# Optimization experiments

Hardware: AMD Instinct MI355X
Metric: run time of the kernel (lower is better)

## Reference

```python
import jax, jax.numpy as jnp
import numpy as np
from jax import lax

B, S, T = 16, 256, 800
V, D, M, H = 256, 512, 80, 1024
NH = 4; HD = D // NH; EH = 256  # encoder LSTM hidden per direction


def setup_inputs() -> dict:
    key = jax.random.key(0)
    it = iter(jax.random.split(key, 40))
    def rn(shape, s=0.05):
        return jax.random.normal(next(it), shape, jnp.float32) * s
    return dict(
        text_inputs=jax.random.randint(next(it), (B, S), 0, V),
        mel_targets=jax.random.normal(next(it), (B, T, M), jnp.float32),
        emb=rn((V, D), 0.1),
        conv_w=rn((3, D, D, 5)), conv_b=rn((3, D)),
        bn_gamma=jnp.ones((3, D)), bn_beta=jnp.zeros((3, D)),
        bn_mean=rn((3, D)), bn_var=jnp.ones((3, D)),
        enc_Wih_f=rn((4 * EH, D)), enc_Whh_f=rn((4 * EH, EH)), enc_b_f=rn((4 * EH,)),
        enc_Wih_b=rn((4 * EH, D)), enc_Whh_b=rn((4 * EH, EH)), enc_b_b=rn((4 * EH,)),
        Wq=rn((D, M)), bq=rn((D,)), Wk=rn((D, D)), bk=rn((D,)),
        Wv=rn((D, D)), bv=rn((D,)), Wo=rn((D, D)), bo=rn((D,)),
        dec_Wih1=rn((4 * H, D + M)), dec_b1=rn((4 * H,)),
        dec_Wih2=rn((4 * H, H)), dec_b2=rn((4 * H,)),
        mel_W=rn((M, H)), mel_b=rn((M,)),
        stop_W=rn((1, H)), stop_b=rn((1,)),
    )


def _lstm_cell_zero(x, Wih, b):
    # single-step LSTM cell from zero (h, c); original resets state every timestep
    g = x @ Wih.T + b
    i, f, gg, o = jnp.split(g, 4, axis=-1)
    c = jax.nn.sigmoid(i) * jnp.tanh(gg)  # c0 = 0 -> forget gate contributes nothing
    return jax.nn.sigmoid(o) * jnp.tanh(c)


def _lstm_scan(xs, Wih, Whh, b, hdim, reverse):
    # xs: (S, B, in); PyTorch gate order i,f,g,o
    def step(carry, xt):
        h, c = carry
        g = xt @ Wih.T + h @ Whh.T + b
        i, f, gg, o = jnp.split(g, 4, axis=-1)
        c = jax.nn.sigmoid(f) * c + jax.nn.sigmoid(i) * jnp.tanh(gg)
        h = jax.nn.sigmoid(o) * jnp.tanh(c)
        return (h, c), h
    z = jnp.zeros((xs.shape[1], hdim), xs.dtype)
    _, hs = lax.scan(step, (z, z), xs, reverse=reverse)
    return hs


def reference(text_inputs, mel_targets, emb, conv_w, conv_b, bn_gamma, bn_beta, bn_mean, bn_var, enc_Wih_f, enc_Whh_f, enc_b_f, enc_Wih_b, enc_Whh_b, enc_b_b, Wq, bq, Wk, bk, Wv, bv, Wo, bo, dec_Wih1, dec_b1, dec_Wih2, dec_b2, mel_W, mel_b, stop_W, stop_b):
    b_, t_, m_ = mel_targets.shape
    # ---- encoder ----
    x = emb[text_inputs].transpose(0, 2, 1)  # (B, D, S)
    for i in range(conv_w.shape[0]):
        x = lax.conv_general_dilated(x, conv_w[i], (1,), [(2, 2)], dimension_numbers=('NCH', 'OIH', 'NCH')) + conv_b[i][None, :, None]
        x = bn_gamma[i][None, :, None] * (x - bn_mean[i][None, :, None]) * lax.rsqrt(bn_var[i][None, :, None] + 1e-5) + bn_beta[i][None, :, None]
        x = jax.nn.relu(x)  # dropout in eval mode -> identity
    xs = x.transpose(2, 0, 1)  # (S, B, D)
    hf = _lstm_scan(xs, enc_Wih_f, enc_Whh_f, enc_b_f, EH, False)
    hb = _lstm_scan(xs, enc_Wih_b, enc_Whh_b, enc_b_b, EH, True)
    enc = jnp.concatenate([hf, hb], -1).transpose(1, 0, 2)  # (B, S, D)
    # ---- decoder (teacher forcing): per-step query = previous mel frame ----
    dec_in = jnp.concatenate([jnp.zeros((b_, 1, m_), mel_targets.dtype), mel_targets[:, :-1]], axis=1)  # (B, T, M)
    q = (dec_in @ Wq.T + bq).reshape(b_, t_, NH, HD)
    k = (enc @ Wk.T + bk).reshape(b_, -1, NH, HD)
    v = (enc @ Wv.T + bv).reshape(b_, -1, NH, HD)
    scores = jnp.einsum('bqhd,bkhd->bhqk', q, k) * (1.0 / np.sqrt(HD)).astype(np.float32)
    attn = jax.nn.softmax(scores, axis=-1)
    ctx = jnp.einsum('bhqk,bkhd->bqhd', attn, v).reshape(b_, t_, D) @ Wo.T + bo
    xcat = jnp.concatenate([ctx, dec_in], axis=-1)  # (B, T, D+M)
    # original re-inits decoder LSTM state each timestep -> stateless per-step cells
    h1 = _lstm_cell_zero(xcat, dec_Wih1, dec_b1)
    h2 = _lstm_cell_zero(h1, dec_Wih2, dec_b2)
    mel = h2 @ mel_W.T + mel_b      # (B, T, 80)
    stop = h2 @ stop_W.T + stop_b   # (B, T, 1) - logits (no sigmoid in training path)
    return mel, stop
```

## Files before the change

### kernel.cpp

```cpp
#include <hip/hip_runtime.h>
#include <hip/hip_bf16.h>
#include <math.h>

#define B_ 16
#define S_ 256
#define T_ 800
#define V_ 256
#define D_ 512
#define M_ 80
#define H_ 1024
#define NH_ 4
#define HD_ 128
#define EH_ 256

using bf16x8 = __attribute__((ext_vector_type(8))) short;
using f32x4  = __attribute__((ext_vector_type(4))) float;
typedef _Float16 half8 __attribute__((ext_vector_type(8)));

__device__ __forceinline__ float sigf(float x) { return 1.f / (1.f + __expf(-x)); }
__device__ __forceinline__ float tanhfast(float x) {
    float e = __expf(2.f * x);
    return 1.f - 2.f / (e + 1.f);
}

__device__ __forceinline__ unsigned short f2bf(float f) {
    unsigned int u = __float_as_uint(f);
    unsigned int r = (u + 0x7FFFu + ((u >> 16) & 1u)) >> 16;
    return (unsigned short)r;
}
__device__ __forceinline__ float bf2f(unsigned short u) {
    return __uint_as_float(((unsigned int)u) << 16);
}
__device__ __forceinline__ unsigned short h2u(_Float16 x) {
    union { _Float16 f; unsigned short u; } c; c.f = x; return c.u;
}

__device__ __forceinline__ void gl_lds16(const unsigned short* g, unsigned short* l) {
    __builtin_amdgcn_global_load_lds((const __attribute__((address_space(1))) void*)g,
                                     (__attribute__((address_space(3))) void*)l, 16, 0, 0);
}

__global__ __launch_bounds__(256) void gemm_mfma(
    const unsigned short* __restrict__ A, const unsigned short* __restrict__ Bw,
    void* __restrict__ Cv, const float* __restrict__ bias,
    int M, int N, int K, int ldc, int epi,
    const float* __restrict__ cb, const float* __restrict__ gam,
    const float* __restrict__ bet, const float* __restrict__ mu,
    const float* __restrict__ va)
{
    __shared__ unsigned short As[4096];
    __shared__ unsigned short Bs[4096];
    const int tid = threadIdx.x, w = tid >> 6, lane = tid & 63;
    const int bm = blockIdx.y * 128, bn = blockIdx.x * 128;
    const int wr = w >> 1, wc = w & 1;

    f32x4 acc[4][4];
#pragma unroll
    for (int m = 0; m < 4; ++m)
#pragma unroll
        for (int n = 0; n < 4; ++n) acc[m][n] = (f32x4){0.f, 0.f, 0.f, 0.f};

    const int r0 = w * 16 + (lane >> 2);
    const int k8 = (lane & 3) * 8;
    const unsigned short* Ag = A + (size_t)(bm + r0) * K + k8;
    const unsigned short* Bg = Bw + (size_t)(bn + r0) * K + k8;
    unsigned short* Al = As + w * 512;
    unsigned short* Bl = Bs + w * 512;

    for (int k0 = 0; k0 < K; k0 += 32) {
        __syncthreads();
        gl_lds16(Ag + k0, Al);
        gl_lds16(Ag + (size_t)64 * K + k0, Al + 2048);
        gl_lds16(Bg + k0, Bl);
        gl_lds16(Bg + (size_t)64 * K + k0, Bl + 2048);
        __syncthreads();
        bf16x8 a[4], b[4];
#pragma unroll
        for (int m = 0; m < 4; ++m)
            a[m] = *(const bf16x8*)(As + (wr * 64 + m * 16 + (lane & 15)) * 32 + (lane >> 4) * 8);
#pragma unroll
        for (int n = 0; n < 4; ++n)
            b[n] = *(const bf16x8*)(Bs + (wc * 64 + n * 16 + (lane & 15)) * 32 + (lane >> 4) * 8);
#pragma unroll
        for (int m = 0; m < 4; ++m)
#pragma unroll
            for (int n = 0; n < 4; ++n)
                acc[m][n] = __builtin_amdgcn_mfma_f32_16x16x32_bf16(a[m], b[n], acc[m][n], 0, 0, 0);
    }

    const int cr = (lane >> 4) * 4, ccol = lane & 15;
#pragma unroll
    for (int m = 0; m < 4; ++m)
#pragma unroll
        for (int n = 0; n < 4; ++n) {
            const int col = bn + wc * 64 + n * 16 + ccol;
            const float bv = (bias && !(epi == 4 && col >= 80)) ? bias[col] : 0.f;
#pragma unroll
            for (int j = 0; j < 4; ++j) {
                const int row = bm + wr * 64 + m * 16 + cr + j;
                float v = acc[m][n][j] + bv;
                if (epi == 1) {
                    float x = v + cb[col];
                    v = fmaxf(0.f, gam[col] * (x - mu[col]) * rsqrtf(va[col] + 1e-5f) + bet[col]);
                }
                if (epi == 2) {
                    ((unsigned short*)Cv)[(size_t)row * ldc + col] = f2bf(v);
                } else if (epi == 3) {
                    const int bb2 = row >> 8, ss = row & 255, hh = col >> 7, dd = col & 127;
                    ((unsigned short*)Cv)[((size_t)(bb2 * 4 + hh) * 128 + dd) * 256 + ss] = f2bf(v);
                } else if (epi == 4) {
                    if (col < 80) ((float*)Cv)[(size_t)row * ldc + col] = v;
                } else {
                    ((float*)Cv)[(size_t)row * ldc + col] = v;
                }
            }
        }
}

__global__ __launch_bounds__(256) void attn_qksm(
    const unsigned short* __restrict__ q, const unsigned short* __restrict__ k,
    unsigned short* __restrict__ probs)
{
    __shared__ unsigned short As[2048];
    __shared__ unsigned short Bs[8192];
    __shared__ float redm[64][4];
    __shared__ float reds[64][4];
    const int tid = threadIdx.x, wid = tid >> 6, lane = tid & 63;
    const int l15 = lane & 15, bq = lane >> 4;
    const int bm = blockIdx.x * 64;
    const int z = blockIdx.y, b = z >> 2, h = z & 3;

    const unsigned short* A  = q + ((size_t)b * T_) * 512 + h * 128;
    const unsigned short* Bw = k + ((size_t)b * S_) * 512 + h * 128;

    f32x4 acc[4][4];
#pragma unroll
    for (int m = 0; m < 4; ++m)
#pragma unroll
        for (int n = 0; n < 4; ++n) acc[m][n] = (f32x4){0.f, 0.f, 0.f, 0.f};

    const int r0 = wid * 16 + (lane >> 2);
    const int k8 = (lane & 3) * 8;

    for (int k0 = 0; k0 < 128; k0 += 32) {
        __syncthreads();
        gl_lds16(A + (size_t)(bm + r0) * 512 + k0 + k8, As + wid * 512);
        gl_lds16(Bw + (size_t)r0 * 512 + k0 + k8,          Bs + wid * 512);
        gl_lds16(Bw + (size_t)(64 + r0) * 512 + k0 + k8,   Bs + 2048 + wid * 512);
        gl_lds16(Bw + (size_t)(128 + r0) * 512 + k0 + k8,  Bs + 4096 + wid * 512);
        gl_lds16(Bw + (size_t)(192 + r0) * 512 + k0 + k8,  Bs + 6144 + wid * 512);
        __syncthreads();
        bf16x8 a[4], bb[4];
#pragma unroll
        for (int m = 0; m < 4; ++m)
            a[m] = *(const bf16x8*)(As + (m * 16 + l15) * 32 + bq * 8);
#pragma unroll
        for (int n = 0; n < 4; ++n)
            bb[n] = *(const bf16x8*)(Bs + (wid * 64 + n * 16 + l15) * 32 + bq * 8);
#pragma unroll
        for (int m = 0; m < 4; ++m)
#pragma unroll
            for (int n = 0; n < 4; ++n)
                acc[m][n] = __builtin_amdgcn_mfma_f32_16x16x32_bf16(a[m], bb[n], acc[m][n], 0, 0, 0);
    }

    const int cr = (lane >> 4) * 4, ccol = lane & 15;
    const float SC = 0.08838834764831843f;

    float lmax[4][4];
#pragma unroll
    for (int m = 0; m < 4; ++m)
#pragma unroll
        for (int j = 0; j < 4; ++j) {
            float v = fmaxf(fmaxf(acc[m][0][j], acc[m][1][j]),
                            fmaxf(acc[m][2][j], acc[m][3][j]));
#pragma unroll
            for (int off = 1; off < 16; off <<= 1) v = fmaxf(v, __shfl_xor(v, off));
            lmax[m][j] = v;
            if (ccol == 0) redm[m * 16 + cr + j][wid] = v;
        }
    __syncthreads();
    float lsum[4][4];
#pragma unroll
    for (int m = 0; m < 4; ++m)
#pragma unroll
        for (int j = 0; j < 4; ++j) {
            const int r = m * 16 + cr + j;
            float mx = fmaxf(fmaxf(redm[r][0], redm[r][1]), fmaxf(redm[r][2], redm[r][3]));
            lmax[m][j] = mx;
            float s = 0.f;
#pragma unroll
            for (int n = 0; n < 4; ++n) {
                float p = __expf((acc[m][n][j] - mx) * SC);
                acc[m][n][j] = p;
                s += p;
            }
#pragma unroll
            for (int off = 1; off < 16; off <<= 1) s += __shfl_xor(s, off);
            lsum[m][j] = s;
            if (ccol == 0) reds[r][wid] = s;
        }
    __syncthreads();
#pragma unroll
    for (int m = 0; m < 4; ++m)
#pragma unroll
        for (int j = 0; j < 4; ++j) {
            const int r = m * 16 + cr + j;
            const int row = bm + r;
            if (row >= T_) continue;
            const float inv = 1.f / (reds[r][0] + reds[r][1] + reds[r][2] + reds[r][3]);
#pragma unroll
            for (int n = 0; n < 4; ++n)
                probs[((size_t)z * T_ + row) * 256 + wid * 64 + n * 16 + ccol] =
                    f2bf(acc[m][n][j] * inv);
        }
}

__global__ __launch_bounds__(256) void attn_pv(
    const unsigned short* __restrict__ probs, const unsigned short* __restrict__ vT,
    unsigned short* __restrict__ ctx)
{
    __shared__ unsigned short As[4096];
    __shared__ unsigned short Bs[4096];
    const int tid = threadIdx.x, w = tid >> 6, lane = tid & 63;
    const int bm = blockIdx.y * 128;
    const int z = blockIdx.z, b = z >> 2, h = z & 3;
    const int wr = w >> 1, wc = w & 1;

    const unsigned short* A  = probs + (size_t)z * T_ * 256;
    const unsigned short* Bw = vT + (size_t)z * 128 * 256;

    f32x4 acc[4][4];
#pragma unroll
    for (int m = 0; m < 4; ++m)
#pragma unroll
        for (int n = 0; n < 4; ++n) acc[m][n] = (f32x4){0.f, 0.f, 0.f, 0.f};

    const int r0 = w * 16 + (lane >> 2);
    const int k8 = (lane & 3) * 8;
    const unsigned short* Ag = A + (size_t)(bm + r0) * 256 + k8;
    const unsigned short* Bg = Bw + (size_t)r0 * 256 + k8;
    unsigned short* Al = As + w * 512;
    unsigned short* Bl = Bs + w * 512;

    for (int k0 = 0; k0 < 256; k0 += 32) {
        __syncthreads();
        gl_lds16(Ag + k0, Al);
        gl_lds16(Ag + (size_t)64 * 256 + k0, Al + 2048);
        gl_lds16(Bg + k0, Bl);
        gl_lds16(Bg + (size_t)64 * 256 + k0, Bl + 2048);
        __syncthreads();
        bf16x8 a[4], bfr[4];
#pragma unroll
        for (int m = 0; m < 4; ++m)
            a[m] = *(const bf16x8*)(As + (wr * 64 + m * 16 + (lane & 15)) * 32 + (lane >> 4) * 8);
#pragma unroll
        for (int n = 0; n < 4; ++n)
            bfr[n] = *(const bf16x8*)(Bs + (wc * 64 + n * 16 + (lane & 15)) * 32 + (lane >> 4) * 8);
#pragma unroll
        for (int m = 0; m < 4; ++m)
#pragma unroll
            for (int n = 0; n < 4; ++n)
                acc[m][n] = __builtin_amdgcn_mfma_f32_16x16x32_bf16(a[m], bfr[n], acc[m][n], 0, 0, 0);
    }

    const int cr = (lane >> 4) * 4, ccol = lane & 15;
#pragma unroll
    for (int m = 0; m < 4; ++m)
#pragma unroll
        for (int n = 0; n < 4; ++n) {
            const int col = wc * 64 + n * 16 + ccol;
#pragma unroll
            for (int j = 0; j < 4; ++j) {
                const int row = bm + wr * 64 + m * 16 + cr + j;
                if (row < T_)
                    ctx[((size_t)b * T_ + row) * 512 + h * 128 + col] = f2bf(acc[m][n][j]);
            }
        }
}

__global__ void embed_k(const int* __restrict__ txt, const float* __restrict__ emb,
                        float* __restrict__ xs)
{
    int idx = blockIdx.x * 256 + threadIdx.x;
    if (idx >= B_ * S_ * D_) return;
    int bs = idx >> 9, dd = idx & 511;
    xs[idx] = emb[(size_t)txt[bs] * D_ + dd];
}

__global__ void im2col_bf(const float* __restrict__ in, unsigned short* __restrict__ out)
{
    int idx = blockIdx.x * 256 + threadIdx.x;
    if (idx >= B_ * S_ * 2560) return;
    int r = idx / 2560, cc = idx % 2560;
    int din = cc / 5, kk = cc % 5;
    int b = r >> 8, s = r & 255;
    int sp = s + kk - 2;
    float v = (sp >= 0 && sp < S_) ? in[((size_t)b * S_ + sp) * D_ + din] : 0.f;
    out[idx] = f2bf(v);
}

__global__ void transp_bf(const float* __restrict__ in, unsigned short* __restrict__ out)
{
    int idx = blockIdx.x * 256 + threadIdx.x;
    if (idx >= B_ * S_ * D_) return;
    int d = idx & 511;
    int sb = idx >> 9;
    int s = sb >> 4, b = sb & 15;
    out[idx] = f2bf(in[((size_t)b * S_ + s) * D_ + d]);
}

__global__ void hist2enc(const _Float16* __restrict__ hist, unsigned short* __restrict__ enc)
{
    int idx = blockIdx.x * 256 + threadIdx.x;
    if (idx >= B_ * S_ * D_) return;
    int d = idx & 511;
    int bs = idx >> 9;
    int b = bs >> 8, s = bs & 255;
    int dir = d >> 8, hid = d & 255;
    enc[idx] = f2bf((float)hist[(((size_t)(dir * 16 + b) * 256 + s) * 256) + hid]);
}

__global__ void cvt_all(
    const float* __restrict__ conv_w, const float* __restrict__ Wih_f,
    const float* __restrict__ Wih_b, const float* __restrict__ Wk,
    const float* __restrict__ Wv, const float* __restrict__ Wq,
    const float* __restrict__ Wo, const float* __restrict__ Wih1,
    const float* __restrict__ Wih2, const float* __restrict__ melW,
    unsigned short* __restrict__ cWc, unsigned short* __restrict__ cWif,
    unsigned short* __restrict__ cWib, unsigned short* __restrict__ cWk,
    unsigned short* __restrict__ cWv, unsigned short* __restrict__ cWq,
    unsigned short* __restrict__ cWo, unsigned short* __restrict__ cW1,
    unsigned short* __restrict__ cW2, unsigned short* __restrict__ cWm)
{
    int idx = blockIdx.x * 256 + threadIdx.x;
    if (idx < 3932160) { cWc[idx] = f2bf(conv_w[idx]); return; }
    idx -= 3932160;
    if (idx < 524288) { cWif[idx] = f2bf(Wih_f[idx]); return; }
    idx -= 524288;
    if (idx < 524288) { cWib[idx] = f2bf(Wih_b[idx]); return; }
    idx -= 524288;
    if (idx < 262144) { cWk[idx] = f2bf(Wk[idx]); return; }
    idx -= 262144;
    if (idx < 262144) { cWv[idx] = f2bf(Wv[idx]); return; }
    idx -= 262144;
    if (idx < 49152) {
        int r = idx / 96, k = idx - r * 96;
        cWq[idx] = (k < 80) ? f2bf(Wq[(size_t)r * 80 + k]) : 0;
        return;
    }
    idx -= 49152;
    if (idx < 262144) { cWo[idx] = f2bf(Wo[idx]); return; }
    idx -= 262144;
    if (idx < 1867776) {
        int n = idx / 608, k = idx - n * 608;
        int orig = (n < 1024) ? n : n + 1024;
        cW1[idx] = (k < 592) ? f2bf(Wih1[(size_t)orig * 592 + k]) : 0;
        return;
    }
    idx -= 1867776;
    if (idx < 3145728) {
        int n = idx >> 10, k = idx & 1023;
        int orig = (n < 1024) ? n : n + 1024;
        cW2[idx] = f2bf(Wih2[(size_t)orig * 1024 + k]);
        return;
    }
    idx -= 3145728;
    if (idx < 131072) {
        int r = idx >> 10, k = idx & 1023;
        cWm[idx] = (r < 80) ? f2bf(melW[(size_t)r * 1024 + k]) : 0;
        return;
    }
}

__global__ void decin_k2(const float* __restrict__ mel, unsigned short* __restrict__ din,
                         unsigned short* __restrict__ xcat)
{
    int idx = blockIdx.x * 256 + threadIdx.x;
    if (idx >= B_ * T_ * 96) return;
    int r = idx / 96, j = idx - r * 96;
    int b = r / T_, t = r - b * T_;
    float v = (j < M_ && t > 0) ? mel[((size_t)b * T_ + t - 1) * M_ + j] : 0.f;
    unsigned short bv = f2bf(v);
    din[(size_t)r * 96 + j] = bv;
    xcat[(size_t)r * 608 + 512 + j] = bv;
}

__global__ void dec_cellb2(const unsigned short* __restrict__ g, const float* __restrict__ b,
                           unsigned short* __restrict__ h, int rows)
{
    int idx = blockIdx.x * 256 + threadIdx.x;
    if (idx >= rows * 512) return;
    int r = idx >> 9, j2 = (idx & 511) * 2;
    const unsigned short* gr = g + (size_t)r * 3072;
    ushort2 vi = *(const ushort2*)(gr + j2);
    ushort2 vg = *(const ushort2*)(gr + 1024 + j2);
    ushort2 vo = *(const ushort2*)(gr + 2048 + j2);
    float i0 = sigf(bf2f(vi.x) + b[j2]),          i1 = sigf(bf2f(vi.y) + b[j2 + 1]);
    float g0 = tanhfast(bf2f(vg.x) + b[2048 + j2]), g1 = tanhfast(bf2f(vg.y) + b[2048 + j2 + 1]);
    float o0 = sigf(bf2f(vo.x) + b[3072 + j2]),   o1 = sigf(bf2f(vo.y) + b[3072 + j2 + 1]);
    ushort2 o;
    o.x = f2bf(o0 * tanhfast(i0 * g0));
    o.y = f2bf(o1 * tanhfast(i1 * g1));
    *(ushort2*)(h + (size_t)r * 1024 + j2) = o;
}

__global__ __launch_bounds__(256) void stop_head(
    const unsigned short* __restrict__ h2, const float* __restrict__ sw,
    const float* __restrict__ sb, float* __restrict__ out)
{
    int row = blockIdx.x * 4 + (threadIdx.x >> 6);
    int lane = threadIdx.x & 63;
    const unsigned short* hr = h2 + (size_t)row * H_;
    float acc = 0.f;
#pragma unroll
    for (int i = 0; i < H_; i += 64) acc += bf2f(hr[i + lane]) * sw[i + lane];
    for (int off = 32; off; off >>= 1) acc += __shfl_xor(acc, off);
    if (lane == 0) out[row] = acc + sb[0];
}

__global__ __launch_bounds__(1024, 4) void lstm_persist9(
    const float* __restrict__ gi_f, const float* __restrict__ gi_b,
    const float* __restrict__ Wf, const float* __restrict__ Wb,
    _Float16* __restrict__ hist,
    unsigned long long* __restrict__ hstage)
{
    const int blk = blockIdx.x;
    const int dir = blk >> 1, half = blk & 1;
    const float* gi = dir ? gi_b : gi_f;
    const float* W  = dir ? Wb : Wf;
    const int tid = threadIdx.x, wid = tid >> 6, lane = tid & 63;
    const int l15 = lane & 15, q = lane >> 4;
    const int half4 = half * 4, ph4 = (half ^ 1) * 4;

    __shared__ _Float16 h_lds[16][264];
    __shared__ float exch[512][17];

    half8 wOA[4], wPA[4], wOB[4], wPB[4];
    {
        const int gt0 = wid >> 3, hb0 = wid & 7;
        const int gt1 = (wid + 16) >> 3;
        const float* wr0 = W + (size_t)(gt0 * 256 + half * 128 + hb0 * 16 + l15) * 256;
        const float* wr1 = W + (size_t)(gt1 * 256 + half * 128 + hb0 * 16 + l15) * 256;
#pragma unroll
        for (int i = 0; i < 4; ++i) {
            const int kO = (half4 + i) * 32 + q * 8;
            const int kP = (ph4 + i) * 32 + q * 8;
            half8 a, b, c, d;
#pragma unroll
            for (int j = 0; j < 8; ++j) {
                a[j] = (_Float16)wr0[kO + j];
                b[j] = (_Float16)wr0[kP + j];
                c[j] = (_Float16)wr1[kO + j];
                d[j] = (_Float16)wr1[kP + j];
            }
            wOA[i] = a; wPA[i] = b; wOB[i] = c; wPB[i] = d;
        }
    }
    for (int i = tid; i < 16 * 264; i += 1024) ((_Float16*)h_lds)[i] = (_Float16)0.f;
    for (int i = tid; i < 512 * 17; i += 1024) ((float*)exch)[i] = 0.f;

    const int hid = tid & 127;
    const int ba  = tid >> 7;
    const int bb  = ba + 8;
    const int gh  = half * 128 + hid;
    const int pc  = (half ^ 1) * 128 + hid;
    float c0 = 0.f, c1 = 0.f;

    const int exr0 = (wid >> 3) * 128 + (wid & 7) * 16 + l15;
    const int exr1 = ((wid + 16) >> 3) * 128 + (wid & 7) * 16 + l15;

    const int own_base = ((dir * 2 + half) * 8 + ba) * 128 + hid;
    const int par_base = ((dir * 2 + (half ^ 1)) * 8 + ba) * 128 + hid;

    float gp0[4], gp1[4];
    {
        const int s0 = dir ? 255 : 0;
        const float* g0 = gi + ((size_t)s0 * 16 + ba) * 1024 + gh;
        const float* g1 = gi + ((size_t)s0 * 16 + bb) * 1024 + gh;
#pragma unroll
        for (int g2 = 0; g2 < 4; ++g2) { gp0[g2] = g0[g2 * 256]; gp1[g2] = g1[g2 * 256]; }
    }
    __syncthreads();

    for (int step = 0; step < 256; ++step) {
        const int s = dir ? (255 - step) : step;
        const unsigned int tag = (unsigned int)(step + 1);
        const int slot = (step & 1) * 4096;

        float h0, h1;
        {
            float xi = exch[hid][ba] + gp0[0];
            float xf = exch[128 + hid][ba] + gp0[1];
            float xg = exch[256 + hid][ba] + gp0[2];
            float xo = exch[384 + hid][ba] + gp0[3];
            float ig = sigf(xi), fg = sigf(xf), gg = tanhfast(xg), og = sigf(xo);
            c0 = fg * c0 + ig * gg; h0 = og * tanhfast(c0);
            xi = exch[hid][bb] + gp1[0];
            xf = exch[128 + hid][bb] + gp1[1];
            xg = exch[256 + hid][bb] + gp1[2];
            xo = exch[384 + hid][bb] + gp1[3];
            ig = sigf(xi); fg = sigf(xf); gg = tanhfast(xg); og = sigf(xo);
            c1 = fg * c1 + ig * gg; h1 = og * tanhfast(c1);
        }
        {
            unsigned int d32 = (unsigned int)h2u((_Float16)h0) |
                               ((unsigned int)h2u((_Float16)h1) << 16);
            unsigned long long wv = ((unsigned long long)tag << 32) | d32;
            __hip_atomic_store(&hstage[slot + own_base], wv,
                               __ATOMIC_RELAXED, __HIP_MEMORY_SCOPE_AGENT);
        }
        h_lds[ba][gh] = (_Float16)h0;
        h_lds[bb][gh] = (_Float16)h1;
        hist[(((size_t)(dir * 16 + ba) * 256 + s) * 256) + gh] = (_Float16)h0;
        hist[(((size_t)(dir * 16 + bb) * 256 + s) * 256) + gh] = (_Float16)h1;
        if (step < 255) {
            const int s2 = dir ? (254 - step) : (step + 1);
            const float* g0 = gi + ((size_t)s2 * 16 + ba) * 1024 + gh;
            const float* g1 = gi + ((size_t)s2 * 16 + bb) * 1024 + gh;
#pragma unroll
            for (int g2 = 0; g2 < 4; ++g2) { gp0[g2] = g0[g2 * 256]; gp1[g2] = g1[g2 * 256]; }
        }
        __syncthreads();

        if (step < 255) {
            f32x4 acc0 = (f32x4){0.f, 0.f, 0.f, 0.f};
            f32x4 acc1 = (f32x4){0.f, 0.f, 0.f, 0.f};
            const _Float16* hrow = &h_lds[l15][0];
#pragma unroll
            for (int i = 0; i < 4; ++i) {
                half8 a = *(const half8*)(hrow + (half4 + i) * 32 + q * 8);
                acc0 = __builtin_amdgcn_mfma_f32_16x16x32_f16(a, wOA[i], acc0, 0, 0, 0);
                acc1 = __builtin_amdgcn_mfma_f32_16x16x32_f16(a, wOB[i], acc1, 0, 0, 0);
            }
            {
                unsigned long long pv;
                do {
                    pv = __hip_atomic_load(&hstage[slot + par_base],
                                           __ATOMIC_RELAXED, __HIP_MEMORY_SCOPE_AGENT);
                } while ((unsigned int)(pv >> 32) != tag);
                unsigned int d32 = (unsigned int)pv;
                *(unsigned short*)&h_lds[ba][pc] = (unsigned short)(d32 & 0xFFFF);
                *(unsigned short*)&h_lds[bb][pc] = (unsigned short)(d32 >> 16);
            }
            __syncthreads();
#pragma unroll
            for (int i = 0; i < 4; ++i) {
                half8 a = *(const half8*)(hrow + (ph4 + i) * 32 + q * 8);
                acc0 = __builtin_amdgcn_mfma_f32_16x16x32_f16(a, wPA[i], acc0, 0, 0, 0);
                acc1 = __builtin_amdgcn_mfma_f32_16x16x32_f16(a, wPB[i], acc1, 0, 0, 0);
            }
            *(f32x4*)&exch[exr0][q * 4] = acc0;
            *(f32x4*)&exch[exr1][q * 4] = acc1;
            __syncthreads();
        }
    }
}

static inline void launch_mfma(hipStream_t st, const unsigned short* A, const unsigned short* B,
                               void* C, const float* bias, int M, int N, int K, int ldc, int epi = 0,
                               const float* cb = nullptr, const float* gam = nullptr,
                               const float* bet = nullptr, const float* mu = nullptr,
                               const float* va = nullptr)
{
    dim3 grid(N / 128, M / 128);
    gemm_mfma<<<grid, 256, 0, st>>>(A, B, C, bias, M, N, K, ldc, epi, cb, gam, bet, mu, va);
}

extern "C" void kernel_launch(void* const* d_in, const int* in_sizes, int n_in,
                              void* d_out, int out_size, void* d_ws, size_t ws_size,
                              hipStream_t stream)
{
    const int*   text   = (const int*)d_in[0];
    const float* mel_t  = (const float*)d_in[1];
    const float* emb    = (const float*)d_in[2];
    const float* conv_w = (const float*)d_in[3];
    const float* conv_b = (const float*)d_in[4];
    const float* bn_g   = (const float*)d_in[5];
    const float* bn_b   = (const float*)d_in[6];
    const float* bn_m   = (const float*)d_in[7];
    const float* bn_v   = (const float*)d_in[8];
    const float* Wih_f  = (const float*)d_in[9];
    const float* Whh_f  = (const float*)d_in[10];
    const float* b_f    = (const float*)d_in[11];
    const float* Wih_b  = (const float*)d_in[12];
    const float* Whh_b  = (const float*)d_in[13];
    const float* b_b    = (const float*)d_in[14];
    const float* Wq     = (const float*)d_in[15];
    const float* bq     = (const float*)d_in[16];
    const float* Wk     = (const float*)d_in[17];
    const float* bk     = (const float*)d_in[18];
    const float* Wv     = (const float*)d_in[19];
    const float* bv     = (const float*)d_in[20];
    const float* Wo     = (const float*)d_in[21];
    const float* bo     = (const float*)d_in[22];
    const float* Wih1   = (const float*)d_in[23];
    const float* b1     = (const float*)d_in[24];
    const float* Wih2   = (const float*)d_in[25];
    const float* b2     = (const float*)d_in[26];
    const float* melW   = (const float*)d_in[27];
    const float* melb   = (const float*)d_in[28];
    const float* stopW  = (const float*)d_in[29];
    const float* stopb  = (const float*)d_in[30];
    float* out = (float*)d_out;
    (void)in_sizes; (void)n_in; (void)out_size; (void)ws_size;

    float* ws = (float*)d_ws;
    float* big  = ws;
    float* pool = ws + 13107200;

    unsigned long long* hstage = (unsigned long long*)(ws + 6000000);

    float*          gi_f   = pool + 0;
    float*          gi_b   = pool + 4194304;
    unsigned short* enc_bf = (unsigned short*)(pool + 8388608);
    float*          P0     = pool + 9437184;
    float*          P1     = pool + 11534336;
    unsigned short* xsT    = (unsigned short*)(pool + 13631488);
    _Float16*       hist   = (_Float16*)(pool + 14155776);
    unsigned short* kbf    = (unsigned short*)(pool + 0);
    unsigned short* vT     = (unsigned short*)(pool + 1048576);
    unsigned short* qbf    = (unsigned short*)(pool + 2097152);
    unsigned short* probs  = (unsigned short*)(pool + 9437184);
    unsigned short* dinb   = (unsigned short*)(pool + 16008192);
    unsigned short* ctxb   = (unsigned short*)(pool + 16622592);
    unsigned short* gatesb = (unsigned short*)(pool + 0);
    unsigned short* h2b    = (unsigned short*)big;
    unsigned short* h1b    = (unsigned short*)(big + 4000000);
    unsigned short* xcat   = (unsigned short*)(pool + 19899392);
    float*          WB     = pool + 23790592;
    unsigned short* cWc  = (unsigned short*)(WB + 0);
    unsigned short* cWif = (unsigned short*)(WB + 1966080);
    unsigned short* cWib = (unsigned short*)(WB + 2228224);
    unsigned short* cWk  = (unsigned short*)(WB + 2490368);
    unsigned short* cWv  = (unsigned short*)(WB + 2621440);
    unsigned short* cWq  = (unsigned short*)(WB + 2752512);
    unsigned short* cWo  = (unsigned short*)(WB + 2777088);
    unsigned short* cW1  = (unsigned short*)(WB + 2908160);
    unsigned short* cW2  = (unsigned short*)(WB + 3842048);
    unsigned short* cWm  = (unsigned short*)(WB + 5414912);

    auto ceil256 = [](int n) { return (n + 255) / 256; };

    hipMemsetAsync(hstage, 0, 8192 * 8, stream);

    cvt_all<<<ceil256(10960896), 256, 0, stream>>>(
        conv_w, Wih_f, Wih_b, Wk, Wv, Wq, Wo, Wih1, Wih2, melW,
        cWc, cWif, cWib, cWk, cWv, cWq, cWo, cW1, cW2, cWm);

    embed_k<<<ceil256(B_ * S_ * D_), 256, 0, stream>>>(text, emb, P0);
    float* cin = P0;
    float* cout = P1;
    for (int l = 0; l < 3; ++l) {
        im2col_bf<<<ceil256(B_ * S_ * 2560), 256, 0, stream>>>(cin, (unsigned short*)big);
        launch_mfma(stream, (unsigned short*)big, cWc + (size_t)l * 512 * 2560,
                    cout, nullptr, B_ * S_, 512, 2560, 512, 1,
                    conv_b + l * 512, bn_g + l * 512, bn_b + l * 512, bn_m + l * 512, bn_v + l * 512);
        float* tmp = cin; cin = cout; cout = tmp;
    }
    transp_bf<<<ceil256(B_ * S_ * D_), 256, 0, stream>>>(cin, xsT);

    launch_mfma(stream, xsT, cWif, gi_f, b_f, S_ * B_, 1024, 512, 1024);
    launch_mfma(stream, xsT, cWib, gi_b, b_b, S_ * B_, 1024, 512, 1024);
    lstm_persist9<<<4, 1024, 0, stream>>>(gi_f, gi_b, Whh_f, Whh_b, hist, hstage);
    hist2enc<<<ceil256(B_ * S_ * D_), 256, 0, stream>>>(hist, enc_bf);

    launch_mfma(stream, enc_bf, cWk, kbf, bk, B_ * S_, 512, 512, 512, 2);
    launch_mfma(stream, enc_bf, cWv, vT, bv, B_ * S_, 512, 512, 0, 3);
    decin_k2<<<ceil256(B_ * T_ * 96), 256, 0, stream>>>(mel_t, dinb, xcat);
    launch_mfma(stream, dinb, cWq, qbf, bq, B_ * T_, 512, 96, 512, 2);

    attn_qksm<<<dim3(13, 64), 256, 0, stream>>>(qbf, kbf, probs);
    attn_pv<<<dim3(1, 7, 64), 256, 0, stream>>>(probs, vT, ctxb);

    launch_mfma(stream, ctxb, cWo, xcat, bo, B_ * T_, 512, 512, 608, 2);

    launch_mfma(stream, xcat, cW1, gatesb, nullptr, B_ * T_, 3072, 608, 3072, 2);
    dec_cellb2<<<ceil256(B_ * T_ * 512), 256, 0, stream>>>(gatesb, b1, h1b, B_ * T_);
    launch_mfma(stream, h1b, cW2, gatesb, nullptr, B_ * T_, 3072, 1024, 3072, 2);
    dec_cellb2<<<ceil256(B_ * T_ * 512), 256, 0, stream>>>(gatesb, b2, h2b, B_ * T_);

    launch_mfma(stream, h2b, cWm, out, melb, B_ * T_, 128, 1024, 80, 4);
    stop_head<<<(B_ * T_) / 4, 256, 0, stream>>>(h2b, stopW, stopb, out + (size_t)B_ * T_ * M_);
}
```

Measured before the change: 1.576 ms.

## Fuse decoder LSTM gate GEMMs with cell activation epilogue

Replaces the two decoder gate GEMM plus elementwise cell kernel pairs with a single fused kernel per layer. Each block computes the i, g and o gate tiles for the same 128 hidden columns in sequence, keeping the earlier gates packed as bf16 in registers, then applies the LSTM cell and writes h directly. This removes the write and re-read of the 12800x3072 bf16 gate buffer and two launches. In exchange the kernel uses a simple non-pipelined GEMM loop with a large register footprint that may lower occupancy.

```diff
diff --git a/kernel.cpp b/kernel.cpp
--- a/kernel.cpp
+++ b/kernel.cpp
@@ -117,6 +117,93 @@
         }
 }
 
+__global__ __launch_bounds__(256) void dec_fused(
+    const unsigned short* __restrict__ A, const unsigned short* __restrict__ Bw,
+    const float* __restrict__ bias, unsigned short* __restrict__ hout,
+    int K)
+{
+    __shared__ unsigned short As[4096];
+    __shared__ unsigned short Bs[4096];
+    const int tid = threadIdx.x, w = tid >> 6, lane = tid & 63;
+    const int bnh = blockIdx.x * 128, bm = blockIdx.y * 128;
+    const int wr = w >> 1, wc = w & 1;
+    const int r0 = w * 16 + (lane >> 2);
+    const int k8 = (lane & 3) * 8;
+    const int cr = (lane >> 4) * 4, ccol = lane & 15;
+
+    unsigned int ig[4][4][4];
+    f32x4 acc[4][4];
+
+    const unsigned short* Ag = A + (size_t)(bm + r0) * K + k8;
+    unsigned short* Al = As + w * 512;
+    unsigned short* Bl = Bs + w * 512;
+
+    for (int gate = 0; gate < 3; ++gate) {
+#pragma unroll
+        for (int m = 0; m < 4; ++m)
+#pragma unroll
+            for (int n = 0; n < 4; ++n) acc[m][n] = (f32x4){0.f, 0.f, 0.f, 0.f};
+
+        const unsigned short* Bg = Bw + (size_t)(gate * 1024 + bnh + r0) * K + k8;
+        for (int k0 = 0; k0 < K; k0 += 32) {
+            __syncthreads();
+            gl_lds16(Ag + k0, Al);
+            gl_lds16(Ag + (size_t)64 * K + k0, Al + 2048);
+            gl_lds16(Bg + k0, Bl);
+            gl_lds16(Bg + (size_t)64 * K + k0, Bl + 2048);
+            __syncthreads();
+            bf16x8 a[4], b[4];
+#pragma unroll
+            for (int m = 0; m < 4; ++m)
+                a[m] = *(const bf16x8*)(As + (wr * 64 + m * 16 + (lane & 15)) * 32 + (lane >> 4) * 8);
+#pragma unroll
+            for (int n = 0; n < 4; ++n)
+                b[n] = *(const bf16x8*)(Bs + (wc * 64 + n * 16 + (lane & 15)) * 32 + (lane >> 4) * 8);
+#pragma unroll
+            for (int m = 0; m < 4; ++m)
+#pragma unroll
+                for (int n = 0; n < 4; ++n)
+                    acc[m][n] = __builtin_amdgcn_mfma_f32_16x16x32_bf16(a[m], b[n], acc[m][n], 0, 0, 0);
+        }
+
+        if (gate == 0) {
+#pragma unroll
+            for (int m = 0; m < 4; ++m)
+#pragma unroll
+                for (int n = 0; n < 4; ++n)
+#pragma unroll
+                    for (int j = 0; j < 4; ++j)
+                        ig[m][n][j] = (unsigned int)f2bf(acc[m][n][j]);
+        } else if (gate == 1) {
+#pragma unroll
+            for (int m = 0; m < 4; ++m)
+#pragma unroll
+                for (int n = 0; n < 4; ++n)
+#pragma unroll
+                    for (int j = 0; j < 4; ++j)
+                        ig[m][n][j] |= (unsigned int)f2bf(acc[m][n][j]) << 16;
+        } else {
+#pragma unroll
+            for (int m = 0; m < 4; ++m)
+#pragma unroll
+                for (int n = 0; n < 4; ++n) {
+                    const int jh = bnh + wc * 64 + n * 16 + ccol;
+                    const float bi = bias[jh];
+                    const float bg = bias[2048 + jh];
+                    const float bo = bias[3072 + jh];
+#pragma unroll
+                    for (int j = 0; j < 4; ++j) {
+                        const int row = bm + wr * 64 + m * 16 + cr + j;
+                        float iv = sigf(bf2f((unsigned short)(ig[m][n][j] & 0xFFFF)) + bi);
+                        float gv = tanhfast(bf2f((unsigned short)(ig[m][n][j] >> 16)) + bg);
+                        float ov = sigf(acc[m][n][j] + bo);
+                        hout[(size_t)row * 1024 + jh] = f2bf(ov * tanhfast(iv * gv));
+                    }
+                }
+        }
+    }
+}
+
 __global__ __launch_bounds__(256) void attn_qksm(
     const unsigned short* __restrict__ q, const unsigned short* __restrict__ k,
     unsigned short* __restrict__ probs)
@@ -384,25 +471,6 @@
     unsigned short bv = f2bf(v);
     din[(size_t)r * 96 + j] = bv;
     xcat[(size_t)r * 608 + 512 + j] = bv;
-}
-
-__global__ void dec_cellb2(const unsigned short* __restrict__ g, const float* __restrict__ b,
-                           unsigned short* __restrict__ h, int rows)
-{
-    int idx = blockIdx.x * 256 + threadIdx.x;
-    if (idx >= rows * 512) return;
-    int r = idx >> 9, j2 = (idx & 511) * 2;
-    const unsigned short* gr = g + (size_t)r * 3072;
-    ushort2 vi = *(const ushort2*)(gr + j2);
-    ushort2 vg = *(const ushort2*)(gr + 1024 + j2);
-    ushort2 vo = *(const ushort2*)(gr + 2048 + j2);
-    float i0 = sigf(bf2f(vi.x) + b[j2]),          i1 = sigf(bf2f(vi.y) + b[j2 + 1]);
-    float g0 = tanhfast(bf2f(vg.x) + b[2048 + j2]), g1 = tanhfast(bf2f(vg.y) + b[2048 + j2 + 1]);
-    float o0 = sigf(bf2f(vo.x) + b[3072 + j2]),   o1 = sigf(bf2f(vo.y) + b[3072 + j2 + 1]);
-    ushort2 o;
-    o.x = f2bf(o0 * tanhfast(i0 * g0));
-    o.y = f2bf(o1 * tanhfast(i1 * g1));
-    *(ushort2*)(h + (size_t)r * 1024 + j2) = o;
 }
 
 __global__ __launch_bounds__(256) void stop_head(
@@ -624,7 +692,6 @@
     unsigned short* probs  = (unsigned short*)(pool + 9437184);
     unsigned short* dinb   = (unsigned short*)(pool + 16008192);
     unsigned short* ctxb   = (unsigned short*)(pool + 16622592);
-    unsigned short* gatesb = (unsigned short*)(pool + 0);
     unsigned short* h2b    = (unsigned short*)big;
     unsigned short* h1b    = (unsigned short*)(big + 4000000);
     unsigned short* xcat   = (unsigned short*)(pool + 19899392);
@@ -675,10 +742,11 @@
 
     launch_mfma(stream, ctxb, cWo, xcat, bo, B_ * T_, 512, 512, 608, 2);
 
-    launch_mfma(stream, xcat, cW1, gatesb, nullptr, B_ * T_, 3072, 608, 3072, 2);
-    dec_cellb2<<<ceil256(B_ * T_ * 512), 256, 0, stream>>>(gatesb, b1, h1b, B_ * T_);
-    launch_mfma(stream, h1b, cW2, gatesb, nullptr, B_ * T_, 3072, 1024, 3072, 2);
-    dec_cellb2<<<ceil256(B_ * T_ * 512), 256, 0, stream>>>(gatesb, b2, h2b, B_ * T_);
+    {
+        dim3 grid(8, B_ * T_ / 128);
+        dec_fused<<<grid, 256, 0, stream>>>(xcat, cW1, b1, h1b, 608);
+        dec_fused<<<grid, 256, 0, stream>>>(h1b, cW2, b2, h2b, 1024);
+    }
 
     launch_mfma(stream, h2b, cWm, out, melb, B_ * T_, 128, 1024, 80, 4);
     stop_head<<<(B_ * T_) / 4, 256, 0, stream>>>(h2b, stopW, stopb, out + (size_t)B_ * T_ * M_);
```

Result: slower. 1.763 ms (+11.9%).
